# Performance work log

Hardware: AMD Instinct MI355X
Metric: run time of the kernel (lower is better)

Reference implementation:

```python
import jax, jax.numpy as jnp
import numpy as np

HEADS = 8
NEG_SLOPE = 0.2


def _layer_norm(x, g, b, eps=1e-5):
    mu = x.mean(-1, keepdims=True)
    var = ((x - mu) ** 2).mean(-1, keepdims=True)
    return (x - mu) / jnp.sqrt(var + eps) * g + b


def setup_inputs() -> dict:
    key = jax.random.key(0)
    ks = jax.random.split(key, 24)
    N, E, H, L = 512, 260000, 256, 4
    s = 0.05
    return dict(
        x=jax.random.normal(ks[0], (N, 1), jnp.float32),
        edge_index=jax.random.randint(ks[1], (2, E), 0, N),
        edge_attr=jax.random.uniform(ks[2], (E, 3), jnp.float32),
        emb_W=jax.random.normal(ks[3], (1, H)) * s,
        emb_b=jnp.zeros((H,)),
        Wl=jax.random.normal(ks[4], (L, H, H)) * s,
        bl=jnp.zeros((L, H)),
        Wr=jax.random.normal(ks[5], (L, H, H)) * s,
        br=jnp.zeros((L, H)),
        We=jax.random.normal(ks[6], (L, 3, H)) * s,
        att=jax.random.normal(ks[7], (L, HEADS, H // HEADS)) * s,
        gb=jnp.zeros((L, H)),
        ln_g=jnp.ones((L, H)),
        ln_b=jnp.zeros((L, H)),
        p1_W=jax.random.normal(ks[8], (2 * H, H)) * s,
        p1_b=jnp.zeros((H,)),
        p2_W=jax.random.normal(ks[9], (H, H // 2)) * s,
        p2_b=jnp.zeros((H // 2,)),
        p3_W=jax.random.normal(ks[10], (H // 2, 1)) * s,
        p3_b=jnp.zeros((1,)),
        v1_W=jax.random.normal(ks[11], (2 * H, H)) * s,
        v1_b=jnp.zeros((H,)),
        v2_W=jax.random.normal(ks[12], (H, 1)) * s,
        v2_b=jnp.zeros((1,)),
        coupling=jnp.asarray(1.0, jnp.float32),
    )


def reference(x, edge_index, edge_attr, emb_W, emb_b, Wl, bl, Wr, br, We, att,
              gb, ln_g, ln_b, p1_W, p1_b, p2_W, p2_b, p3_W, p3_b,
              v1_W, v1_b, v2_W, v2_b, coupling):
    N = x.shape[0]
    E = edge_attr.shape[0]
    L = Wl.shape[0]
    C = Wl.shape[-1] // HEADS
    src, dst = edge_index[0], edge_index[1]

    # PyG GATv2Conv adds self-loops with edge_attr fill_value='mean'
    # (mean of incoming edge_attr per destination node).
    sums = jax.ops.segment_sum(edge_attr, dst, num_segments=N)
    cnt = jax.ops.segment_sum(jnp.ones((E,), edge_attr.dtype), dst, num_segments=N)
    self_attr = sums / jnp.maximum(cnt, 1.0)[:, None]
    loop = jnp.arange(N)
    src_f = jnp.concatenate([src, loop])            # [E+N]
    dst_f = jnp.concatenate([dst, loop])
    ea_f = jnp.concatenate([edge_attr, self_attr])  # [E+N, 3]

    h = x @ emb_W + emb_b                           # [N, H]
    for l in range(L):
        res = h
        xl = (h @ Wl[l] + bl[l]).reshape(N, HEADS, C)
        xr = (h @ Wr[l] + br[l]).reshape(N, HEADS, C)
        ee = (ea_f @ We[l]).reshape(-1, HEADS, C)
        # GATv2 scoring: leaky_relu(x_l[src]+x_r[dst]+edge) . att
        m = jax.nn.leaky_relu(xl[src_f] + xr[dst_f] + ee, NEG_SLOPE)
        alpha = jnp.einsum('ehc,hc->eh', m, att[l])
        amax = jax.ops.segment_max(alpha, dst_f, num_segments=N)
        alpha = jnp.exp(alpha - amax[dst_f])
        denom = jax.ops.segment_sum(alpha, dst_f, num_segments=N)
        alpha = alpha / denom[dst_f]
        out = jax.ops.segment_sum(xl[src_f] * alpha[..., None], dst_f,
                                  num_segments=N).reshape(N, HEADS * C) + gb[l]
        h = jax.nn.relu(_layer_norm(out + res, ln_g[l], ln_b[l]))

    # graph-level representation (single graph, batch=None branch)
    graph_repr = jnp.concatenate([h.mean(0, keepdims=True),
                                  h.max(0, keepdims=True)], axis=1)  # [1, 2H]

    # all-pairs edge representations (i < j)
    iu, ju = jnp.triu_indices(N, k=1)
    er = jnp.concatenate([h[iu], h[ju]], axis=1)    # [N(N-1)/2, 2H]
    p = jax.nn.relu(er @ p1_W + p1_b)
    p = jax.nn.relu(p @ p2_W + p2_b)
    policy_logits = (p @ p3_W + p3_b).squeeze(-1)   # [N(N-1)/2]

    v = jax.nn.relu(graph_repr @ v1_W + v1_b)
    value = (v @ v2_W + v2_b).squeeze(-1)           # [1]

    # Potts energy: per-color degree-squared approximation of triangles
    colors = jnp.argmax(edge_attr, axis=1)
    energy = jnp.asarray(0.0, h.dtype)
    for c in (1, 2):
        w = (colors == c).astype(h.dtype)
        deg = (jax.ops.segment_sum(w, src, num_segments=N)
               + jax.ops.segment_sum(w, dst, num_segments=N))
        energy = energy + (deg ** 2).sum() / (2.0 * N)
    energy = energy * coupling

    return policy_logits, value, energy
```

## Files before the change

kernel.cpp:

```cpp
#include <hip/hip_runtime.h>
#include <math.h>

#define HDIM 256
#define NHEADS 8
#define NEG 0.2f
#define NB 256
#define SEG 4

typedef float f32x4 __attribute__((ext_vector_type(4)));
typedef _Float16 f16x8 __attribute__((ext_vector_type(8)));
typedef __fp16 fp16v2 __attribute__((ext_vector_type(2)));

__global__ __launch_bounds__(256) void edge_part(
    const int* __restrict__ ei, const float* __restrict__ ea, int E, int CH,
    int* __restrict__ pcnt, float* __restrict__ psum, int* __restrict__ pcol) {
  __shared__ int   lcnt[512];
  __shared__ float ls0[512], ls1[512], ls2[512];
  __shared__ int   lcol[1024];
  int t = threadIdx.x, b = blockIdx.x;
  for (int n = t; n < 512; n += 256) {
    lcnt[n] = 0; ls0[n] = 0.f; ls1[n] = 0.f; ls2[n] = 0.f;
    lcol[n] = 0; lcol[512 + n] = 0;
  }
  __syncthreads();
  int e0 = b * CH, e1 = min(E, e0 + CH);
  for (int e = e0 + t; e < e1; e += 256) {
    int src = ei[e], dst = ei[E + e];
    float a0 = ea[3*e], a1 = ea[3*e+1], a2 = ea[3*e+2];
    atomicAdd(&lcnt[dst], 1);
    atomicAdd(&ls0[dst], a0);
    atomicAdd(&ls1[dst], a1);
    atomicAdd(&ls2[dst], a2);
    int idx = 0; float best = a0;
    if (a1 > best) { best = a1; idx = 1; }
    if (a2 > best) { idx = 2; }
    if (idx) {
      int o = (idx - 1) << 9;
      atomicAdd(&lcol[o + src], 1);
      atomicAdd(&lcol[o + dst], 1);
    }
  }
  __syncthreads();
  for (int n = t; n < 512; n += 256) {
    pcnt[b*512 + n] = lcnt[n];
    psum[(size_t)(0*NB + b)*512 + n] = ls0[n];
    psum[(size_t)(1*NB + b)*512 + n] = ls1[n];
    psum[(size_t)(2*NB + b)*512 + n] = ls2[n];
    pcol[(size_t)(0*NB + b)*512 + n] = lcol[n];
    pcol[(size_t)(1*NB + b)*512 + n] = lcol[512 + n];
  }
}

__global__ __launch_bounds__(256) void red_kernel(
    const int* __restrict__ pcnt, const float* __restrict__ psum,
    const int* __restrict__ pcol,
    int* __restrict__ cnt, float* __restrict__ sred, int* __restrict__ dred,
    int* __restrict__ pbase) {
  int q = blockIdx.x >> 1;
  int n = (blockIdx.x & 1)*256 + threadIdx.x;
  if (q == 0) {
    int run = 0;
#pragma unroll 8
    for (int b = 0; b < NB; ++b) {
      int v = pcnt[b*512 + n];
      pbase[b*512 + n] = run;
      run += v;
    }
    cnt[n] = run;
  } else if (q <= 3) {
    int qq = q - 1;
    float s = 0.f;
#pragma unroll 8
    for (int b = 0; b < NB; ++b) s += psum[(size_t)(qq*NB + b)*512 + n];
    sred[qq*512 + n] = s;
  } else {
    int qq = q - 4;
    int s = 0;
#pragma unroll 8
    for (int b = 0; b < NB; ++b) s += pcol[(size_t)(qq*NB + b)*512 + n];
    dred[qq*512 + n] = s;
  }
}

__global__ __launch_bounds__(512) void scan2(
    const int* __restrict__ cnt, const float* __restrict__ sred,
    const int* __restrict__ dred, int N,
    int* __restrict__ rowp, float4* __restrict__ csr,
    const float* __restrict__ coupling, float* __restrict__ eout) {
  int t = threadIdx.x;
  int c = (t < N) ? cnt[t] : 0;
  __shared__ int sbuf[512];
  int v = (t < N) ? (c + 1) : 0;
  sbuf[t] = v;
  __syncthreads();
  for (int off = 1; off < 512; off <<= 1) {
    int add = (t >= off) ? sbuf[t - off] : 0;
    __syncthreads();
    sbuf[t] += add;
    __syncthreads();
  }
  int incl = sbuf[t], excl = incl - v;
  if (t < N) {
    rowp[t] = excl;
    if (t == N - 1) rowp[N] = incl;
    float inv = 1.f / fmaxf((float)c, 1.f);
    csr[excl] = make_float4(sred[t]*inv, sred[512 + t]*inv, sred[1024 + t]*inv,
                            __int_as_float(t));
  }
  float e = 0.f;
  if (t < N) {
    float d1 = (float)dred[t], d2 = (float)dred[512 + t];
    e = d1*d1 + d2*d2;
  }
#pragma unroll
  for (int off = 1; off < 64; off <<= 1) e += __shfl_xor(e, off);
  __shared__ float wred[8];
  if ((t & 63) == 0) wred[t >> 6] = e;
  __syncthreads();
  if (t == 0) {
    float s = 0.f;
#pragma unroll
    for (int i = 0; i < 8; ++i) s += wred[i];
    eout[0] = coupling[0] * s / (2.f * (float)N);
  }
}

__global__ __launch_bounds__(256) void scatter2(
    const int* __restrict__ ei, const float* __restrict__ ea, int E, int CH,
    const int* __restrict__ rowp, const int* __restrict__ pbase,
    float4* __restrict__ csr) {
  __shared__ int lofs[512];
  int t = threadIdx.x, b = blockIdx.x;
  for (int n = t; n < 512; n += 256) lofs[n] = 0;
  __syncthreads();
  int e0 = b * CH, e1 = min(E, e0 + CH);
  for (int e = e0 + t; e < e1; e += 256) {
    int src = ei[e], dst = ei[E + e];
    float a0 = ea[3*e], a1 = ea[3*e+1], a2 = ea[3*e+2];
    int lp = atomicAdd(&lofs[dst], 1);
    int pos = rowp[dst] + 1 + pbase[b*512 + dst] + lp;
    csr[pos] = make_float4(a0, a1, a2, __int_as_float(src));
  }
}

__global__ __launch_bounds__(256) void w_prep_all(
    const float* __restrict__ Wl, const float* __restrict__ Wr,
    const float* __restrict__ p1W, const float* __restrict__ W2,
    unsigned short* __restrict__ dst, unsigned short* __restrict__ W2h) {
  int gid = blockIdx.x * 256 + threadIdx.x;
  if (gid < 10*65536) {
    int s = gid >> 16, e = gid & 65535;
    int k = e >> 8, n = e & 255;
    const float* src = (s < 4) ? (Wl + (size_t)s*65536)
                     : (s < 8) ? (Wr + (size_t)(s-4)*65536)
                               : (p1W + (size_t)(s-8)*65536);
    int c = k >> 5, quad = (k >> 3) & 3, kj = k & 7;
    int nt = n >> 4, nl = n & 15;
    int lane = quad*16 + nl;
    _Float16 hv = (_Float16)src[(size_t)k*256 + n];
    dst[(size_t)s*65536 + ((nt*8 + c)*512 + lane*8 + kj)] = *(unsigned short*)&hv;
  } else {
    int e = gid - 10*65536;
    int k = e >> 7, n = e & 127;
    int c = k >> 5, kq = (k >> 3) & 3, kj = k & 7;
    int nt = n >> 4, nl = n & 15;
    int lane = kq*16 + nl;
    _Float16 hv = (_Float16)W2[(size_t)k*128 + n];
    W2h[(size_t)(((c*8 + nt)*64 + lane)*8 + kj)] = *(unsigned short*)&hv;
  }
}

__global__ __launch_bounds__(256) void dual_gemm_mfma(
    const float* __restrict__ Hm,
    const float* __restrict__ x, const float* __restrict__ embW,
    const float* __restrict__ embb,
    const unsigned short* __restrict__ W1h, const unsigned short* __restrict__ W2h,
    const float* __restrict__ b1, const float* __restrict__ b2,
    float* __restrict__ o1, unsigned short* __restrict__ o1h,
    float* __restrict__ o2, unsigned short* __restrict__ o2h) {
  int bx = blockIdx.x, by = blockIdx.y;
  int t = threadIdx.x, w = t >> 6, l = t & 63;
  int quad = l >> 4, nl = l & 15;
  int mt = bx*4 + w;

  const unsigned short* Wh; const float* bias; float* o; unsigned short* oh; int nt;
  bool first = (by < 16);
  if (first) { Wh = W1h; bias = b1; o = o1; oh = o1h; nt = by; }
  else       { Wh = W2h; bias = b2; o = o2; oh = o2h; nt = by - 16; }

  int row = mt*16 + nl;
  const float* Ar = Hm ? (Hm + (size_t)row*HDIM + quad*8) : nullptr;
  float xm = Hm ? 0.f : x[row];
  f32x4 acc = (f32x4){0.f, 0.f, 0.f, 0.f};

#pragma unroll
  for (int c = 0; c < 8; ++c) {
    float4 a0, a1;
    if (Hm) {
      a0 = *(const float4*)(Ar + c*32);
      a1 = *(const float4*)(Ar + c*32 + 4);
    } else {
      int kb = c*32 + quad*8;
      float4 e0 = *(const float4*)(embW + kb);
      float4 e1 = *(const float4*)(embW + kb + 4);
      float4 c0 = *(const float4*)(embb + kb);
      float4 c1 = *(const float4*)(embb + kb + 4);
      a0 = make_float4(fmaf(xm, e0.x, c0.x), fmaf(xm, e0.y, c0.y),
                       fmaf(xm, e0.z, c0.z), fmaf(xm, e0.w, c0.w));
      a1 = make_float4(fmaf(xm, e1.x, c1.x), fmaf(xm, e1.y, c1.y),
                       fmaf(xm, e1.z, c1.z), fmaf(xm, e1.w, c1.w));
    }
    union { f16x8 v8; fp16v2 v2[4]; } u;
    u.v2[0] = __builtin_amdgcn_cvt_pkrtz(a0.x, a0.y);
    u.v2[1] = __builtin_amdgcn_cvt_pkrtz(a0.z, a0.w);
    u.v2[2] = __builtin_amdgcn_cvt_pkrtz(a1.x, a1.y);
    u.v2[3] = __builtin_amdgcn_cvt_pkrtz(a1.z, a1.w);
    f16x8 bfrag = *(const f16x8*)(Wh + (size_t)((nt*8 + c)*512 + l*8));
    acc = __builtin_amdgcn_mfma_f32_16x16x32_f16(u.v8, bfrag, acc, 0, 0, 0);
  }

  int colg = nt*16 + nl;
  float bv = bias ? bias[colg] : 0.f;
#pragma unroll
  for (int r = 0; r < 4; ++r) {
    float val = acc[r] + bv;
    size_t idx = (size_t)(mt*16 + quad*4 + r)*HDIM + colg;
    if (o) o[idx] = val;
    if (oh) {
      _Float16 hv = (_Float16)val;
      oh[idx] = *(unsigned short*)&hv;
    }
  }
}

__global__ __launch_bounds__(256) void attn_gather(
    const unsigned short* __restrict__ xlh, const float* __restrict__ xr,
    const float4* __restrict__ csr, const int* __restrict__ row_start,
    const float* __restrict__ We, const float* __restrict__ att,
    float* __restrict__ pm, float* __restrict__ pl, float* __restrict__ pacc) {
  int nb = blockIdx.x;
  int n = nb >> 2, sgm = nb & (SEG - 1);
  int t = threadIdx.x;
  int g = t >> 5, l = t & 31, hd = l >> 2, qd = l & 3;
  int cb = hd*32 + qd*8;

  float xrv[8], w0[8], w1[8], w2[8], av[8];
#pragma unroll
  for (int j = 0; j < 8; ++j) {
    xrv[j] = xr[(size_t)n*HDIM + cb + j];
    w0[j]  = We[cb + j];
    w1[j]  = We[HDIM + cb + j];
    w2[j]  = We[2*HDIM + cb + j];
    av[j]  = att[cb + j];
  }
  int rs = row_start[n], re = row_start[n+1], len = re - rs;
  int s0 = rs + ((len * sgm) >> 2);
  int s1 = rs + ((len * (sgm + 1)) >> 2);

  float mh = -INFINITY, lh = 0.f;
  float acc[8] = {0.f,0.f,0.f,0.f,0.f,0.f,0.f,0.f};

  int idx = s0 + g;
  if (idx < s1) {
    float4 rec = csr[idx];
    int idx1 = idx + 8;
    float4 rec1 = csr[idx1 < s1 ? idx1 : rs];
    union { f16x8 v8; _Float16 h[8]; } cur, nxt;
    cur.v8 = *(const f16x8*)(xlh + (size_t)__float_as_int(rec.w)*HDIM + cb);
    while (idx < s1) {
      int idx2 = idx1 + 8;
      float4 rec2 = csr[idx2 < s1 ? idx2 : rs];
      nxt.v8 = *(const f16x8*)(xlh +
                (size_t)__float_as_int(rec1.w)*HDIM + cb);
      float xv[8];
#pragma unroll
      for (int j = 0; j < 8; ++j) xv[j] = (float)cur.h[j];
      float partial = 0.f;
#pragma unroll
      for (int j = 0; j < 8; ++j) {
        float m = fmaf(rec.z, w2[j], fmaf(rec.y, w1[j], fmaf(rec.x, w0[j], xrv[j]))) + xv[j];
        m = fmaxf(m, NEG * m);
        partial = fmaf(m, av[j], partial);
      }
      partial += __shfl_xor(partial, 1);
      partial += __shfl_xor(partial, 2);
      if (partial > mh) {
        float sc = __expf(mh - partial);
        lh *= sc;
#pragma unroll
        for (int j = 0; j < 8; ++j) acc[j] *= sc;
        mh = partial;
      }
      float pw = __expf(partial - mh);
      lh += pw;
#pragma unroll
      for (int j = 0; j < 8; ++j) acc[j] = fmaf(pw, xv[j], acc[j]);
      rec = rec1; rec1 = rec2; cur.v8 = nxt.v8;
      idx = idx1; idx1 = idx2;
    }
  }

  __shared__ float lacc[8][HDIM];
  __shared__ float lm[8][NHEADS];
  __shared__ float llv[8][NHEADS];
#pragma unroll
  for (int j = 0; j < 8; ++j) lacc[g][cb + j] = acc[j];
  if (qd == 0) { lm[g][hd] = mh; llv[g][hd] = lh; }
  __syncthreads();

  int c = t, hh = c >> 5;
  float M = -INFINITY;
#pragma unroll
  for (int g2 = 0; g2 < 8; ++g2) M = fmaxf(M, lm[g2][hh]);
  float L = 0.f, o = 0.f;
#pragma unroll
  for (int g2 = 0; g2 < 8; ++g2) {
    float e2 = __expf(lm[g2][hh] - M);
    L = fmaf(llv[g2][hh], e2, L);
    o = fmaf(lacc[g2][c], e2, o);
  }
  pacc[(size_t)nb*HDIM + c] = o;
  if ((c & 31) == 0) {
    pm[nb*NHEADS + hh] = M;
    pl[nb*NHEADS + hh] = L;
  }
}

__global__ __launch_bounds__(256) void attn_merge(
    const float* __restrict__ pm, const float* __restrict__ pl,
    const float* __restrict__ pacc,
    const float* __restrict__ gb, const float* __restrict__ lng,
    const float* __restrict__ lnb,
    const float* __restrict__ h_in,
    const float* __restrict__ x, const float* __restrict__ embW,
    const float* __restrict__ embb,
    float* __restrict__ h_out) {
  int n = blockIdx.x, t = threadIdx.x;
  int c = t, hh = c >> 5;
  float M = -INFINITY;
#pragma unroll
  for (int s = 0; s < SEG; ++s) M = fmaxf(M, pm[(n*SEG + s)*NHEADS + hh]);
  float L = 0.f, o = 0.f;
#pragma unroll
  for (int s = 0; s < SEG; ++s) {
    float e2 = __expf(pm[(n*SEG + s)*NHEADS + hh] - M);
    L = fmaf(pl[(n*SEG + s)*NHEADS + hh], e2, L);
    o = fmaf(pacc[(size_t)(n*SEG + s)*HDIM + c], e2, o);
  }
  float hi = h_in ? h_in[(size_t)n*HDIM + c] : fmaf(x[n], embW[c], embb[c]);
  float val = o / L + gb[c] + hi;

  float s1 = val, s2 = val * val;
#pragma unroll
  for (int off = 1; off < 64; off <<= 1) {
    s1 += __shfl_xor(s1, off);
    s2 += __shfl_xor(s2, off);
  }
  __shared__ float rs1[4], rs2[4];
  if ((t & 63) == 0) { rs1[t >> 6] = s1; rs2[t >> 6] = s2; }
  __syncthreads();
  float S1 = rs1[0] + rs1[1] + rs1[2] + rs1[3];
  float S2 = rs2[0] + rs2[1] + rs2[2] + rs2[3];
  float mu = S1 * (1.f/HDIM);
  float var = S2 * (1.f/HDIM) - mu * mu;
  float y = (val - mu) * rsqrtf(var + 1e-5f);
  y = fmaf(y, lng[c], lnb[c]);
  h_out[(size_t)n*HDIM + c] = fmaxf(y, 0.f);
}

__global__ __launch_bounds__(256, 4) void pair_mfma_kernel(
    const unsigned short* __restrict__ Ah, const unsigned short* __restrict__ Bh,
    const unsigned short* __restrict__ W2h,
    const float* __restrict__ b2, const float* __restrict__ W3,
    const float* __restrict__ b3, float* __restrict__ out, int N) {
  int bb = blockIdx.x;
  int half = bb & 1;
  int b = bb >> 1, ti = 0, rem = 32;
  while (b >= rem) { b -= rem; ti++; rem--; }
  int tj = ti + b;
  int i0 = ti * 16 + half * 8;
  int j0 = tj * 16;

  int t = threadIdx.x;
  int w = t >> 6, l = t & 63;
  int quad = l >> 4, nl = l & 15;

  float b2v[8], w3v[8];
#pragma unroll
  for (int nt = 0; nt < 8; ++nt) {
    b2v[nt] = b2[nt*16 + nl];
    w3v[nt] = W3[nt*16 + nl];
  }

  const unsigned short* Brow = Bh + (size_t)(j0 + nl) * HDIM;
  const unsigned short* Arow0 = Ah + (size_t)(i0 + w*2) * HDIM;
  const _Float16 zero = (_Float16)0.f;

  f32x4 acc[2][8];
#pragma unroll
  for (int a2 = 0; a2 < 2; ++a2)
#pragma unroll
    for (int nt = 0; nt < 8; ++nt) acc[a2][nt] = (f32x4){0.f,0.f,0.f,0.f};

  for (int c = 0; c < 8; ++c) {
    int kb = c*32 + quad*8;
    f16x8 bv = *(const f16x8*)(Brow + kb);

    f16x8 afrag[2];
#pragma unroll
    for (int a2 = 0; a2 < 2; ++a2) {
      f16x8 av = *(const f16x8*)(Arow0 + (size_t)a2*HDIM + kb);
      union { f16x8 v8; _Float16 h[8]; } u;
      u.v8 = av + bv;
#pragma unroll
      for (int j = 0; j < 8; ++j)
        u.h[j] = u.h[j] > zero ? u.h[j] : zero;
      afrag[a2] = u.v8;
    }

#pragma unroll
    for (int nt = 0; nt < 8; ++nt) {
      f16x8 bfrag = *(const f16x8*)(W2h + (size_t)(((c*8 + nt)*64 + l) * 8));
#pragma unroll
      for (int a2 = 0; a2 < 2; ++a2)
        acc[a2][nt] = __builtin_amdgcn_mfma_f32_16x16x32_f16(
            afrag[a2], bfrag, acc[a2][nt], 0, 0, 0);
    }
  }

  float b3v = b3[0];
#pragma unroll
  for (int a2 = 0; a2 < 2; ++a2) {
    int i = i0 + w*2 + a2;
#pragma unroll
    for (int r = 0; r < 4; ++r) {
      float s = 0.f;
#pragma unroll
      for (int nt = 0; nt < 8; ++nt)
        s = fmaf(fmaxf(acc[a2][nt][r] + b2v[nt], 0.f), w3v[nt], s);
      s += __shfl_xor(s, 1);
      s += __shfl_xor(s, 2);
      s += __shfl_xor(s, 4);
      s += __shfl_xor(s, 8);
      if (nl == 0) {
        int j = j0 + quad*4 + r;
        if (i < j)
          out[(size_t)i*(2*N - i - 1)/2 + (j - i - 1)] = s + b3v;
      }
    }
  }
}

__global__ __launch_bounds__(256) void pool_kernel(
    const float* __restrict__ h, float* __restrict__ psums,
    float* __restrict__ pmaxs) {
  int g = blockIdx.x, t = threadIdx.x;
  float s = 0.f, m = -INFINITY;
#pragma unroll
  for (int r = 0; r < 16; ++r) {
    float v = h[(size_t)(g*16 + r)*HDIM + t];
    s += v; m = fmaxf(m, v);
  }
  psums[g*HDIM + t] = s;
  pmaxs[g*HDIM + t] = m;
}

__global__ __launch_bounds__(256) void value1_kernel(
    const float* __restrict__ psums, const float* __restrict__ pmaxs,
    const float* __restrict__ v1W, float* __restrict__ vpart, int N) {
  int b = blockIdx.x, t = threadIdx.x;
  int k0 = b * 16;
  int kk = t >> 4, g = t & 15;
  __shared__ float repr16[16];
  int k = k0 + kk;
  float v;
  if (k < HDIM) {
    v = psums[g*HDIM + k] + psums[(g + 16)*HDIM + k];
    v += __shfl_xor(v, 1); v += __shfl_xor(v, 2);
    v += __shfl_xor(v, 4); v += __shfl_xor(v, 8);
    if (g == 0) repr16[kk] = v / (float)N;
  } else {
    int kc = k - HDIM;
    v = fmaxf(pmaxs[g*HDIM + kc], pmaxs[(g + 16)*HDIM + kc]);
    v = fmaxf(v, __shfl_xor(v, 1)); v = fmaxf(v, __shfl_xor(v, 2));
    v = fmaxf(v, __shfl_xor(v, 4)); v = fmaxf(v, __shfl_xor(v, 8));
    if (g == 0) repr16[kk] = v;
  }
  __syncthreads();
  float pv = 0.f;
#pragma unroll
  for (int q = 0; q < 16; ++q)
    pv = fmaf(repr16[q], v1W[(size_t)(k0 + q)*HDIM + t], pv);
  vpart[b*HDIM + t] = pv;
}

__global__ __launch_bounds__(256) void value2_kernel(
    const float* __restrict__ vpart, const float* __restrict__ v1b,
    const float* __restrict__ v2W, const float* __restrict__ v2b,
    float* __restrict__ out) {
  int t = threadIdx.x;
  float a = 0.f;
#pragma unroll
  for (int g = 0; g < 32; ++g) a += vpart[g*HDIM + t];
  a = fmaxf(a + v1b[t], 0.f);
  float pv = a * v2W[t];
#pragma unroll
  for (int off = 1; off < 64; off <<= 1) pv += __shfl_xor(pv, off);
  __shared__ float wsum[4];
  if ((t & 63) == 0) wsum[t >> 6] = pv;
  __syncthreads();
  if (t == 0) out[0] = wsum[0] + wsum[1] + wsum[2] + wsum[3] + v2b[0];
}

extern "C" void kernel_launch(void* const* d_in, const int* in_sizes, int n_in,
                              void* d_out, int out_size, void* d_ws, size_t ws_size,
                              hipStream_t stream) {
  const float* x    = (const float*)d_in[0];
  const int*   ei   = (const int*)  d_in[1];
  const float* ea   = (const float*)d_in[2];
  const float* embW = (const float*)d_in[3];
  const float* embb = (const float*)d_in[4];
  const float* Wl   = (const float*)d_in[5];
  const float* bl   = (const float*)d_in[6];
  const float* Wr   = (const float*)d_in[7];
  const float* br   = (const float*)d_in[8];
  const float* We   = (const float*)d_in[9];
  const float* att  = (const float*)d_in[10];
  const float* gb   = (const float*)d_in[11];
  const float* lng  = (const float*)d_in[12];
  const float* lnb  = (const float*)d_in[13];
  const float* p1W  = (const float*)d_in[14];
  const float* p1b  = (const float*)d_in[15];
  const float* p2W  = (const float*)d_in[16];
  const float* p2b  = (const float*)d_in[17];
  const float* p3W  = (const float*)d_in[18];
  const float* p3b  = (const float*)d_in[19];
  const float* v1W  = (const float*)d_in[20];
  const float* v1b  = (const float*)d_in[21];
  const float* v2W  = (const float*)d_in[22];
  const float* v2b  = (const float*)d_in[23];
  const float* coup = (const float*)d_in[24];

  int N = in_sizes[0];
  int E = in_sizes[2] / 3;
  float* out = (float*)d_out;
  size_t P = (size_t)N*(N-1)/2;

  char* w = (char*)d_ws;
  int*    rowp = (int*)   (w + 0);
  float*  plS  = (float*) (w + 2560);
  float*  plM  = (float*) (w + 35328);
  float*  vprt = (float*) (w + 68096);
  float4* csr  = (float4*)(w + 101120);
  size_t csr_end = 101120 + (size_t)(E + N) * 16;
  csr_end = (csr_end + 255) & ~(size_t)255;
  float* hA  = (float*)(w + csr_end);
  float* hB  = hA  + (size_t)N*HDIM;
  float* xrb = hB  + (size_t)N*HDIM;
  unsigned short* xlh = (unsigned short*)(xrb + (size_t)N*HDIM);
  unsigned short* Abh = xlh + (size_t)N*HDIM;
  unsigned short* Bbh = Abh + (size_t)N*HDIM;
  unsigned short* W2h = Bbh + (size_t)N*HDIM;
  unsigned short* Whall = W2h + 32768;
  size_t ubase = ((size_t)((char*)(Whall + 10*65536) - w) + 255) & ~(size_t)255;

  char* U = w + ubase;
  int*    pcnt = (int*)   (U + 0);
  float*  psum = (float*) (U + 524288);
  int*    pcol = (int*)   (U + 2097152);
  int*    pbase= (int*)   (U + 3145728);
  int*    cnt  = (int*)   (U + 3670016);
  float*  sred = (float*) (U + 3672064);
  int*    dred = (int*)   (U + 3678208);
  float*  pmv  = (float*) (U + 0);
  float*  plv  = (float*) (U + 65536);
  float*  pacc = (float*) (U + 131072);

  int CH = (E + NB - 1) / NB;
  edge_part<<<NB, 256, 0, stream>>>(ei, ea, E, CH, pcnt, psum, pcol);
  red_kernel<<<12, 256, 0, stream>>>(pcnt, psum, pcol, cnt, sred, dred, pbase);
  scan2<<<1, 512, 0, stream>>>(cnt, sred, dred, N, rowp, csr, coup, out + P + 1);
  scatter2<<<NB, 256, 0, stream>>>(ei, ea, E, CH, rowp, pbase, csr);
  w_prep_all<<<2688, 256, 0, stream>>>(Wl, Wr, p1W, p2W, Whall, W2h);

  float* hin = nullptr;
  float* hout = hB;
  for (int l = 0; l < 4; ++l) {
    dual_gemm_mfma<<<dim3(8, 32), 256, 0, stream>>>(hin, x, embW, embb,
        Whall + (size_t)l*65536, Whall + (size_t)(4 + l)*65536,
        bl + l*HDIM, br + l*HDIM,
        (float*)nullptr, xlh, xrb, (unsigned short*)nullptr);
    attn_gather<<<N*SEG, 256, 0, stream>>>(xlh, xrb, csr, rowp,
        We + (size_t)l*3*HDIM, att + (size_t)l*HDIM, pmv, plv, pacc);
    attn_merge<<<N, 256, 0, stream>>>(pmv, plv, pacc,
        gb + (size_t)l*HDIM, lng + (size_t)l*HDIM, lnb + (size_t)l*HDIM,
        hin, x, embW, embb, hout);
    hin = hout;
    hout = (hout == hB) ? hA : hB;
  }

  dual_gemm_mfma<<<dim3(8, 32), 256, 0, stream>>>(hin, x, embW, embb,
      Whall + (size_t)8*65536, Whall + (size_t)9*65536,
      p1b, (const float*)nullptr,
      (float*)nullptr, Abh, (float*)nullptr, Bbh);

  pair_mfma_kernel<<<1056, 256, 0, stream>>>(Abh, Bbh, W2h, p2b, p3W, p3b, out, N);

  pool_kernel<<<32, 256, 0, stream>>>(hin, plS, plM);
  value1_kernel<<<32, 256, 0, stream>>>(plS, plM, v1W, vprt, N);
  value2_kernel<<<1, 256, 0, stream>>>(vprt, v1b, v2W, v2b, out + P);
}
```

Measured before the change: 308.6 us.

## Build fixed-stride CSR in one pass and do attention messages in packed fp16

The four-kernel CSR build (per-block partials, serial reduction, scan, second scatter pass) becomes one kernel. Each destination node gets a fixed 768-slot bucket, filled using per-block shared counts and global atomics, followed by a small finish kernel. The attention gather now computes messages with packed fp16 vector math and fdot2, reads x_r as fp16, and skips the online-softmax rescale unless the new max exceeds the old by more than 8. The pair kernel's ReLU becomes a vector max. The fixed stride assumes in-degree stays under 767, and fp16 accumulation of messages lowers precision.

```diff
diff --git a/kernel.cpp b/kernel.cpp
--- a/kernel.cpp
+++ b/kernel.cpp
@@ -4,19 +4,35 @@
 #define HDIM 256
 #define NHEADS 8
 #define NEG 0.2f
-#define NB 256
 #define SEG 4
+#define STRIDE 768
 
 typedef float f32x4 __attribute__((ext_vector_type(4)));
 typedef _Float16 f16x8 __attribute__((ext_vector_type(8)));
 typedef __fp16 fp16v2 __attribute__((ext_vector_type(2)));
 
-__global__ __launch_bounds__(256) void edge_part(
+union H8 { f16x8 v8; fp16v2 v2[4]; _Float16 h[8]; };
+
+#if __has_builtin(__builtin_amdgcn_fdot2)
+#define FDOT2(a, b, c) __builtin_amdgcn_fdot2((a), (b), (c), false)
+#else
+__device__ __forceinline__ float FDOT2(fp16v2 a, fp16v2 b, float c) {
+  return fmaf((float)a[1], (float)b[1], fmaf((float)a[0], (float)b[0], c));
+}
+#endif
+
+__global__ __launch_bounds__(256) void zero_k(int* __restrict__ p) {
+  p[blockIdx.x * 256 + threadIdx.x] = 0;
+}
+
+__global__ __launch_bounds__(256) void build_csr(
     const int* __restrict__ ei, const float* __restrict__ ea, int E, int CH,
-    int* __restrict__ pcnt, float* __restrict__ psum, int* __restrict__ pcol) {
+    int* __restrict__ rcnt, float* __restrict__ asum, int* __restrict__ dcol,
+    float4* __restrict__ csr) {
   __shared__ int   lcnt[512];
   __shared__ float ls0[512], ls1[512], ls2[512];
   __shared__ int   lcol[1024];
+  __shared__ int   lbase[512];
   int t = threadIdx.x, b = blockIdx.x;
   for (int n = t; n < 512; n += 256) {
     lcnt[n] = 0; ls0[n] = 0.f; ls1[n] = 0.f; ls2[n] = 0.f;
@@ -24,92 +40,69 @@
   }
   __syncthreads();
   int e0 = b * CH, e1 = min(E, e0 + CH);
-  for (int e = e0 + t; e < e1; e += 256) {
-    int src = ei[e], dst = ei[E + e];
-    float a0 = ea[3*e], a1 = ea[3*e+1], a2 = ea[3*e+2];
-    atomicAdd(&lcnt[dst], 1);
-    atomicAdd(&ls0[dst], a0);
-    atomicAdd(&ls1[dst], a1);
-    atomicAdd(&ls2[dst], a2);
-    int idx = 0; float best = a0;
-    if (a1 > best) { best = a1; idx = 1; }
-    if (a2 > best) { idx = 2; }
-    if (idx) {
-      int o = (idx - 1) << 9;
-      atomicAdd(&lcol[o + src], 1);
-      atomicAdd(&lcol[o + dst], 1);
+
+  int nd[4], ns[4], slot[4];
+  float va0[4], va1[4], va2[4];
+#pragma unroll
+  for (int k = 0; k < 4; ++k) {
+    int e = e0 + t + (k << 8);
+    bool v = e < e1;
+    if (v) {
+      int src = ei[e], dst = ei[E + e];
+      float a0 = ea[3*e], a1 = ea[3*e+1], a2 = ea[3*e+2];
+      nd[k] = dst; ns[k] = src; va0[k] = a0; va1[k] = a1; va2[k] = a2;
+      slot[k] = atomicAdd(&lcnt[dst], 1);
+      atomicAdd(&ls0[dst], a0);
+      atomicAdd(&ls1[dst], a1);
+      atomicAdd(&ls2[dst], a2);
+      int idx = 0; float best = a0;
+      if (a1 > best) { best = a1; idx = 1; }
+      if (a2 > best) { idx = 2; }
+      if (idx) {
+        int o = (idx - 1) << 9;
+        atomicAdd(&lcol[o + src], 1);
+        atomicAdd(&lcol[o + dst], 1);
+      }
+    } else {
+      nd[k] = -1;
     }
   }
   __syncthreads();
   for (int n = t; n < 512; n += 256) {
-    pcnt[b*512 + n] = lcnt[n];
-    psum[(size_t)(0*NB + b)*512 + n] = ls0[n];
-    psum[(size_t)(1*NB + b)*512 + n] = ls1[n];
-    psum[(size_t)(2*NB + b)*512 + n] = ls2[n];
-    pcol[(size_t)(0*NB + b)*512 + n] = lcol[n];
-    pcol[(size_t)(1*NB + b)*512 + n] = lcol[512 + n];
-  }
-}
-
-__global__ __launch_bounds__(256) void red_kernel(
-    const int* __restrict__ pcnt, const float* __restrict__ psum,
-    const int* __restrict__ pcol,
-    int* __restrict__ cnt, float* __restrict__ sred, int* __restrict__ dred,
-    int* __restrict__ pbase) {
-  int q = blockIdx.x >> 1;
-  int n = (blockIdx.x & 1)*256 + threadIdx.x;
-  if (q == 0) {
-    int run = 0;
-#pragma unroll 8
-    for (int b = 0; b < NB; ++b) {
-      int v = pcnt[b*512 + n];
-      pbase[b*512 + n] = run;
-      run += v;
-    }
-    cnt[n] = run;
-  } else if (q <= 3) {
-    int qq = q - 1;
-    float s = 0.f;
-#pragma unroll 8
-    for (int b = 0; b < NB; ++b) s += psum[(size_t)(qq*NB + b)*512 + n];
-    sred[qq*512 + n] = s;
-  } else {
-    int qq = q - 4;
-    int s = 0;
-#pragma unroll 8
-    for (int b = 0; b < NB; ++b) s += pcol[(size_t)(qq*NB + b)*512 + n];
-    dred[qq*512 + n] = s;
-  }
-}
-
-__global__ __launch_bounds__(512) void scan2(
-    const int* __restrict__ cnt, const float* __restrict__ sred,
-    const int* __restrict__ dred, int N,
-    int* __restrict__ rowp, float4* __restrict__ csr,
-    const float* __restrict__ coupling, float* __restrict__ eout) {
+    int c = lcnt[n];
+    if (c) {
+      lbase[n] = atomicAdd(&rcnt[n], c);
+      atomicAdd(&asum[n],        ls0[n]);
+      atomicAdd(&asum[512 + n],  ls1[n]);
+      atomicAdd(&asum[1024 + n], ls2[n]);
+    }
+    int c0 = lcol[n], c1 = lcol[512 + n];
+    if (c0) atomicAdd(&dcol[n], c0);
+    if (c1) atomicAdd(&dcol[512 + n], c1);
+  }
+  __syncthreads();
+#pragma unroll
+  for (int k = 0; k < 4; ++k) {
+    if (nd[k] >= 0) {
+      int pos = nd[k]*STRIDE + 1 + lbase[nd[k]] + slot[k];
+      csr[pos] = make_float4(va0[k], va1[k], va2[k], __int_as_float(ns[k]));
+    }
+  }
+}
+
+__global__ __launch_bounds__(512) void csr_finish(
+    const int* __restrict__ rcnt, const float* __restrict__ asum,
+    const int* __restrict__ dcol, int N,
+    float4* __restrict__ csr, const float* __restrict__ coupling,
+    float* __restrict__ eout) {
   int t = threadIdx.x;
-  int c = (t < N) ? cnt[t] : 0;
-  __shared__ int sbuf[512];
-  int v = (t < N) ? (c + 1) : 0;
-  sbuf[t] = v;
-  __syncthreads();
-  for (int off = 1; off < 512; off <<= 1) {
-    int add = (t >= off) ? sbuf[t - off] : 0;
-    __syncthreads();
-    sbuf[t] += add;
-    __syncthreads();
-  }
-  int incl = sbuf[t], excl = incl - v;
-  if (t < N) {
-    rowp[t] = excl;
-    if (t == N - 1) rowp[N] = incl;
-    float inv = 1.f / fmaxf((float)c, 1.f);
-    csr[excl] = make_float4(sred[t]*inv, sred[512 + t]*inv, sred[1024 + t]*inv,
-                            __int_as_float(t));
-  }
   float e = 0.f;
   if (t < N) {
-    float d1 = (float)dred[t], d2 = (float)dred[512 + t];
+    int c = rcnt[t];
+    float inv = 1.f / fmaxf((float)c, 1.f);
+    csr[(size_t)t*STRIDE] = make_float4(asum[t]*inv, asum[512 + t]*inv,
+                                        asum[1024 + t]*inv, __int_as_float(t));
+    float d1 = (float)dcol[t], d2 = (float)dcol[512 + t];
     e = d1*d1 + d2*d2;
   }
 #pragma unroll
@@ -122,24 +115,6 @@
 #pragma unroll
     for (int i = 0; i < 8; ++i) s += wred[i];
     eout[0] = coupling[0] * s / (2.f * (float)N);
-  }
-}
-
-__global__ __launch_bounds__(256) void scatter2(
-    const int* __restrict__ ei, const float* __restrict__ ea, int E, int CH,
-    const int* __restrict__ rowp, const int* __restrict__ pbase,
-    float4* __restrict__ csr) {
-  __shared__ int lofs[512];
-  int t = threadIdx.x, b = blockIdx.x;
-  for (int n = t; n < 512; n += 256) lofs[n] = 0;
-  __syncthreads();
-  int e0 = b * CH, e1 = min(E, e0 + CH);
-  for (int e = e0 + t; e < e1; e += 256) {
-    int src = ei[e], dst = ei[E + e];
-    float a0 = ea[3*e], a1 = ea[3*e+1], a2 = ea[3*e+2];
-    int lp = atomicAdd(&lofs[dst], 1);
-    int pos = rowp[dst] + 1 + pbase[b*512 + dst] + lp;
-    csr[pos] = make_float4(a0, a1, a2, __int_as_float(src));
   }
 }
 
@@ -234,8 +209,8 @@
 }
 
 __global__ __launch_bounds__(256) void attn_gather(
-    const unsigned short* __restrict__ xlh, const float* __restrict__ xr,
-    const float4* __restrict__ csr, const int* __restrict__ row_start,
+    const unsigned short* __restrict__ xlh, const unsigned short* __restrict__ xrh,
+    const float4* __restrict__ csr, const int* __restrict__ rcnt,
     const float* __restrict__ We, const float* __restrict__ att,
     float* __restrict__ pm, float* __restrict__ pl, float* __restrict__ pacc) {
   int nb = blockIdx.x;
@@ -244,18 +219,20 @@
   int g = t >> 5, l = t & 31, hd = l >> 2, qd = l & 3;
   int cb = hd*32 + qd*8;
 
-  float xrv[8], w0[8], w1[8], w2[8], av[8];
-#pragma unroll
-  for (int j = 0; j < 8; ++j) {
-    xrv[j] = xr[(size_t)n*HDIM + cb + j];
-    w0[j]  = We[cb + j];
-    w1[j]  = We[HDIM + cb + j];
-    w2[j]  = We[2*HDIM + cb + j];
-    av[j]  = att[cb + j];
-  }
-  int rs = row_start[n], re = row_start[n+1], len = re - rs;
-  int s0 = rs + ((len * sgm) >> 2);
-  int s1 = rs + ((len * (sgm + 1)) >> 2);
+  union H8 w0u, w1u, w2u, avu;
+#pragma unroll
+  for (int p = 0; p < 4; ++p) {
+    w0u.v2[p] = __builtin_amdgcn_cvt_pkrtz(We[cb + 2*p],          We[cb + 2*p + 1]);
+    w1u.v2[p] = __builtin_amdgcn_cvt_pkrtz(We[HDIM + cb + 2*p],   We[HDIM + cb + 2*p + 1]);
+    w2u.v2[p] = __builtin_amdgcn_cvt_pkrtz(We[2*HDIM + cb + 2*p], We[2*HDIM + cb + 2*p + 1]);
+    avu.v2[p] = __builtin_amdgcn_cvt_pkrtz(att[cb + 2*p],         att[cb + 2*p + 1]);
+  }
+  f16x8 xr8 = *(const f16x8*)(xrh + (size_t)n*HDIM + cb);
+
+  int base = n * STRIDE;
+  int len = rcnt[n] + 1;
+  int s0 = base + ((len * sgm) >> 2);
+  int s1 = base + ((len * (sgm + 1)) >> 2);
 
   float mh = -INFINITY, lh = 0.f;
   float acc[8] = {0.f,0.f,0.f,0.f,0.f,0.f,0.f,0.f};
@@ -264,27 +241,28 @@
   if (idx < s1) {
     float4 rec = csr[idx];
     int idx1 = idx + 8;
-    float4 rec1 = csr[idx1 < s1 ? idx1 : rs];
-    union { f16x8 v8; _Float16 h[8]; } cur, nxt;
+    float4 rec1 = csr[idx1 < s1 ? idx1 : base];
+    union H8 cur, nxt;
     cur.v8 = *(const f16x8*)(xlh + (size_t)__float_as_int(rec.w)*HDIM + cb);
     while (idx < s1) {
       int idx2 = idx1 + 8;
-      float4 rec2 = csr[idx2 < s1 ? idx2 : rs];
+      float4 rec2 = csr[idx2 < s1 ? idx2 : base];
       nxt.v8 = *(const f16x8*)(xlh +
                 (size_t)__float_as_int(rec1.w)*HDIM + cb);
-      float xv[8];
-#pragma unroll
-      for (int j = 0; j < 8; ++j) xv[j] = (float)cur.h[j];
-      float partial = 0.f;
-#pragma unroll
-      for (int j = 0; j < 8; ++j) {
-        float m = fmaf(rec.z, w2[j], fmaf(rec.y, w1[j], fmaf(rec.x, w0[j], xrv[j]))) + xv[j];
-        m = fmaxf(m, NEG * m);
-        partial = fmaf(m, av[j], partial);
-      }
+      _Float16 hx = (_Float16)rec.x, hy = (_Float16)rec.y, hz = (_Float16)rec.z;
+      f16x8 s = cur.v8 + xr8;
+      s = s + w0u.v8 * hx;
+      s = s + w1u.v8 * hy;
+      s = s + w2u.v8 * hz;
+      union H8 m;
+      m.v8 = __builtin_elementwise_max(s, s * (_Float16)NEG);
+      float partial = FDOT2(m.v2[3], avu.v2[3],
+                      FDOT2(m.v2[2], avu.v2[2],
+                      FDOT2(m.v2[1], avu.v2[1],
+                      FDOT2(m.v2[0], avu.v2[0], 0.f))));
       partial += __shfl_xor(partial, 1);
       partial += __shfl_xor(partial, 2);
-      if (partial > mh) {
+      if (partial - mh > 8.f) {
         float sc = __expf(mh - partial);
         lh *= sc;
 #pragma unroll
@@ -294,7 +272,7 @@
       float pw = __expf(partial - mh);
       lh += pw;
 #pragma unroll
-      for (int j = 0; j < 8; ++j) acc[j] = fmaf(pw, xv[j], acc[j]);
+      for (int j = 0; j < 8; ++j) acc[j] = fmaf(pw, (float)cur.h[j], acc[j]);
       rec = rec1; rec1 = rec2; cur.v8 = nxt.v8;
       idx = idx1; idx1 = idx2;
     }
@@ -394,7 +372,7 @@
 
   const unsigned short* Brow = Bh + (size_t)(j0 + nl) * HDIM;
   const unsigned short* Arow0 = Ah + (size_t)(i0 + w*2) * HDIM;
-  const _Float16 zero = (_Float16)0.f;
+  const f16x8 zv = {};
 
   f32x4 acc[2][8];
 #pragma unroll
@@ -410,12 +388,7 @@
 #pragma unroll
     for (int a2 = 0; a2 < 2; ++a2) {
       f16x8 av = *(const f16x8*)(Arow0 + (size_t)a2*HDIM + kb);
-      union { f16x8 v8; _Float16 h[8]; } u;
-      u.v8 = av + bv;
-#pragma unroll
-      for (int j = 0; j < 8; ++j)
-        u.h[j] = u.h[j] > zero ? u.h[j] : zero;
-      afrag[a2] = u.v8;
+      afrag[a2] = __builtin_elementwise_max(av + bv, zv);
     }
 
 #pragma unroll
@@ -547,40 +520,29 @@
   size_t P = (size_t)N*(N-1)/2;
 
   char* w = (char*)d_ws;
-  int*    rowp = (int*)   (w + 0);
-  float*  plS  = (float*) (w + 2560);
-  float*  plM  = (float*) (w + 35328);
-  float*  vprt = (float*) (w + 68096);
-  float4* csr  = (float4*)(w + 101120);
-  size_t csr_end = 101120 + (size_t)(E + N) * 16;
-  csr_end = (csr_end + 255) & ~(size_t)255;
-  float* hA  = (float*)(w + csr_end);
-  float* hB  = hA  + (size_t)N*HDIM;
-  float* xrb = hB  + (size_t)N*HDIM;
-  unsigned short* xlh = (unsigned short*)(xrb + (size_t)N*HDIM);
-  unsigned short* Abh = xlh + (size_t)N*HDIM;
-  unsigned short* Bbh = Abh + (size_t)N*HDIM;
-  unsigned short* W2h = Bbh + (size_t)N*HDIM;
-  unsigned short* Whall = W2h + 32768;
-  size_t ubase = ((size_t)((char*)(Whall + 10*65536) - w) + 255) & ~(size_t)255;
-
-  char* U = w + ubase;
-  int*    pcnt = (int*)   (U + 0);
-  float*  psum = (float*) (U + 524288);
-  int*    pcol = (int*)   (U + 2097152);
-  int*    pbase= (int*)   (U + 3145728);
-  int*    cnt  = (int*)   (U + 3670016);
-  float*  sred = (float*) (U + 3672064);
-  int*    dred = (int*)   (U + 3678208);
-  float*  pmv  = (float*) (U + 0);
-  float*  plv  = (float*) (U + 65536);
-  float*  pacc = (float*) (U + 131072);
-
-  int CH = (E + NB - 1) / NB;
-  edge_part<<<NB, 256, 0, stream>>>(ei, ea, E, CH, pcnt, psum, pcol);
-  red_kernel<<<12, 256, 0, stream>>>(pcnt, psum, pcol, cnt, sred, dred, pbase);
-  scan2<<<1, 512, 0, stream>>>(cnt, sred, dred, N, rowp, csr, coup, out + P + 1);
-  scatter2<<<NB, 256, 0, stream>>>(ei, ea, E, CH, rowp, pbase, csr);
+  int*    rcnt = (int*)   (w + 0);
+  float*  asum = (float*) (w + 2048);
+  int*    dcol = (int*)   (w + 8192);
+  float*  plS  = (float*) (w + 12288);
+  float*  plM  = (float*) (w + 45056);
+  float*  vprt = (float*) (w + 77824);
+  float4* csr  = (float4*)(w + 110592);
+  float* hA  = (float*)(w + 6402048);
+  float* hB  = (float*)(w + 6926336);
+  unsigned short* xlh = (unsigned short*)(w + 7450624);
+  unsigned short* xrh = (unsigned short*)(w + 7712768);
+  unsigned short* Abh = (unsigned short*)(w + 7974912);
+  unsigned short* Bbh = (unsigned short*)(w + 8237056);
+  unsigned short* W2h = (unsigned short*)(w + 8499200);
+  unsigned short* Whall = (unsigned short*)(w + 8564736);
+  float*  pmv  = (float*) (w + 9875456);
+  float*  plv  = (float*) (w + 9940992);
+  float*  pacc = (float*) (w + 10006528);
+
+  zero_k<<<12, 256, 0, stream>>>(rcnt);
+  int nbB = (E + 1023) >> 10;
+  build_csr<<<nbB, 256, 0, stream>>>(ei, ea, E, 1024, rcnt, asum, dcol, csr);
+  csr_finish<<<1, 512, 0, stream>>>(rcnt, asum, dcol, N, csr, coup, out + P + 1);
   w_prep_all<<<2688, 256, 0, stream>>>(Wl, Wr, p1W, p2W, Whall, W2h);
 
   float* hin = nullptr;
@@ -589,8 +551,8 @@
     dual_gemm_mfma<<<dim3(8, 32), 256, 0, stream>>>(hin, x, embW, embb,
         Whall + (size_t)l*65536, Whall + (size_t)(4 + l)*65536,
         bl + l*HDIM, br + l*HDIM,
-        (float*)nullptr, xlh, xrb, (unsigned short*)nullptr);
-    attn_gather<<<N*SEG, 256, 0, stream>>>(xlh, xrb, csr, rowp,
+        (float*)nullptr, xlh, (float*)nullptr, xrh);
+    attn_gather<<<N*SEG, 256, 0, stream>>>(xlh, xrh, csr, rcnt,
         We + (size_t)l*3*HDIM, att + (size_t)l*HDIM, pmv, plv, pacc);
     attn_merge<<<N, 256, 0, stream>>>(pmv, plv, pacc,
         gb + (size_t)l*HDIM, lng + (size_t)l*HDIM, lnb + (size_t)l*HDIM,
```

Result: faster. 298.1 us (-3.4%).
